# Performance work log

Measured on AMD Instinct MI355X. Metric: run time of the kernel, lower is better.

Reference implementation:

```python
import jax, jax.numpy as jnp
import numpy as np

ALPHA = 0.5
SPLIT_RATIO = 0.5
NUM_HEADS = 12
LN_EPS = 1e-6


def _layernorm(x, g, b):
    m = x.mean(-1, keepdims=True)
    v = ((x - m) ** 2).mean(-1, keepdims=True)
    return (x - m) * jax.lax.rsqrt(v + LN_EPS) * g + b


def setup_inputs() -> dict:
    key = jax.random.key(0)
    ks = jax.random.split(key, 8)
    B, N1, C, L, Hm = 16, 197, 768, 4, 3072
    s = 0.02
    return {
        "x": jax.random.normal(ks[0], (B, N1, C), jnp.float32),
        "glb_cls_attn": jax.random.uniform(ks[1], (B, N1 - 1), jnp.float32),
        "split_w": jax.random.normal(ks[2], (C, 4 * C), jnp.float32) * s,
        "split_b": jnp.zeros((4 * C,), jnp.float32),
        "ln1_g": jnp.ones((L, C), jnp.float32),
        "ln1_b": jnp.zeros((L, C), jnp.float32),
        "qkv_w": jax.random.normal(ks[3], (L, C, 3 * C), jnp.float32) * s,
        "qkv_b": jnp.zeros((L, 3 * C), jnp.float32),
        "proj_w": jax.random.normal(ks[4], (L, C, C), jnp.float32) * s,
        "proj_b": jnp.zeros((L, C), jnp.float32),
        "ln2_g": jnp.ones((L, C), jnp.float32),
        "ln2_b": jnp.zeros((L, C), jnp.float32),
        "fc1_w": jax.random.normal(ks[5], (L, C, Hm), jnp.float32) * s,
        "fc1_b": jnp.zeros((L, Hm), jnp.float32),
        "fc2_w": jax.random.normal(ks[6], (L, Hm, C), jnp.float32) * s,
        "fc2_b": jnp.zeros((L, C), jnp.float32),
    }


def reference(x, glb_cls_attn, split_w, split_b, ln1_g, ln1_b, qkv_w, qkv_b,
              proj_w, proj_b, ln2_g, ln2_b, fc1_w, fc1_b, fc2_w, fc2_b):
    B, _, C = x.shape
    H = NUM_HEADS
    D = C // H
    scale = D ** -0.5

    # --- token split based on global cls attention importance ---
    cls_tok, tokens = x[:, :1], x[:, 1:]
    order = jnp.argsort(-glb_cls_attn, axis=1)  # descending importance
    tokens = jnp.take_along_axis(tokens, order[:, :, None], axis=1)
    n = tokens.shape[1]
    split_n = int(n * SPLIT_RATIO)
    st = tokens[:, :split_n] @ split_w + split_b          # [B, split_n, 4C]
    st = st.reshape(B, split_n * 4, C)                    # each token -> 4 tokens
    x = jnp.concatenate([cls_tok, st, tokens[:, split_n:]], axis=1)
    N = x.shape[1]
    glb = jnp.zeros((B, N - 1), x.dtype)

    def block(carry, p):
        x, g = carry
        g1, b1, qw, qb, pw, pb, g2, b2, w1, bb1, w2, bb2 = p
        h = _layernorm(x, g1, b1)
        qkv = (h @ qw + qb).reshape(B, N, 3, H, D).transpose(2, 0, 3, 1, 4)
        q, k, v = qkv[0], qkv[1], qkv[2]                  # [B,H,N,D]
        attn = jax.nn.softmax(jnp.einsum('bhnd,bhmd->bhnm', q, k) * scale, axis=-1)
        cls_attn = attn[:, :, 0, 1:].mean(axis=1)         # mean over heads, row 0
        o = jnp.einsum('bhnm,bhmd->bhnd', attn, v).transpose(0, 2, 1, 3).reshape(B, N, C)
        x = x + o @ pw + pb
        h2 = _layernorm(x, g2, b2)
        x = x + jax.nn.gelu(h2 @ w1 + bb1, approximate=False) @ w2 + bb2
        g = ALPHA * g + (1.0 - ALPHA) * cls_attn
        return (x, g), None

    (x, glb), _ = jax.lax.scan(
        block, (x, glb),
        (ln1_g, ln1_b, qkv_w, qkv_b, proj_w, proj_b,
         ln2_g, ln2_b, fc1_w, fc1_b, fc2_w, fc2_b))
    return x, glb
```

## Files before the change

kernel.cpp:

```cpp
#include <hip/hip_runtime.h>
#include <math.h>

typedef unsigned short u16;
typedef short s16x8 __attribute__((ext_vector_type(8)));
typedef float f32x4 __attribute__((ext_vector_type(4)));

#define BB 16
#define N1 197
#define NTOK 196
#define SPLITN 98
#define NN 491
#define CC 768
#define H3 2304
#define HM 3072
#define NH 12
#define NL 4
#define BN (BB*NN)
#define MSPLIT (BB*SPLITN)

__device__ __forceinline__ float b2f(u16 u) {
    union { unsigned int i; float f; } x; x.i = ((unsigned int)u) << 16; return x.f;
}
__device__ __forceinline__ u16 f2b(float f) {
    union { float f; unsigned int i; } x; x.f = f;
    unsigned int i = x.i;
    return (u16)((i + 0x7fffu + ((i >> 16) & 1u)) >> 16);
}
__device__ __forceinline__ float ldx(const void* p, long long i, int isf32) {
    return isf32 ? ((const float*)p)[i] : b2f(((const u16*)p)[i]);
}

__device__ __forceinline__ float gelu_fast(float v) {
    float x = v * 0.70710678118654752f;
    float ax = fabsf(x);
    float t = __builtin_amdgcn_rcpf(fmaf(0.3275911f, ax, 1.0f));
    float p = t * fmaf(t, fmaf(t, fmaf(t, fmaf(t, 1.061405429f, -1.453152027f),
                                       1.421413741f), -0.284496736f), 0.254829592f);
    float e = __expf(-ax * ax);
    float er = fmaf(-p, e, 1.0f);
    er = copysignf(er, x);
    return 0.5f * v * (1.0f + er);
}

__device__ __forceinline__ void gload_lds16(const u16* g, u16* l) {
    __builtin_amdgcn_global_load_lds(
        (const __attribute__((address_space(1))) unsigned int*)g,
        (__attribute__((address_space(3))) unsigned int*)l,
        16, 0, 0);
}

__global__ void detect_k(const void* __restrict__ ln1_g, int* __restrict__ flag) {
    unsigned int w = ((const unsigned int*)ln1_g)[0];
    *flag = (w == 0x3F800000u) ? 1 : 0;
}

__global__ void zero_out_k(u16* __restrict__ out, long long n) {
    long long idx = (long long)blockIdx.x * 256 + threadIdx.x;
    if (idx < n) out[idx] = 0;
}

__global__ void zero_glb_k(float* __restrict__ glb) {
    int idx = blockIdx.x * 256 + threadIdx.x;
    if (idx < BB * (NN - 1)) glb[idx] = 0.0f;
}

__global__ void sort_k(const void* __restrict__ g, int* __restrict__ order,
                       const int* __restrict__ dflag) {
    __shared__ float v[256];
    int isf32 = *dflag;
    int b = blockIdx.x, t = threadIdx.x;
    float vv = -1e30f;
    if (t < NTOK) {
        vv = ldx(g, (long long)b * NTOK + t, isf32);
        if (!(vv == vv)) vv = -1e30f;
    }
    v[t] = vv;
    __syncthreads();
    if (t < NTOK) {
        float mv = v[t]; int r = 0;
        for (int j = 0; j < NTOK; j++) {
            float vj = v[j];
            if (vj > mv || (vj == mv && j < t)) r++;
        }
        order[b * NTOK + r] = t;
    }
}

__device__ __forceinline__ int clamp_tok(int tok) {
    return (tok < 0) ? 0 : (tok > NTOK - 1 ? NTOK - 1 : tok);
}

__global__ void gather_split_k(const void* __restrict__ x_in, const int* __restrict__ order,
                               u16* __restrict__ Asp, const int* __restrict__ dflag) {
    int isf32 = *dflag;
    long long idx = (long long)blockIdx.x * 256 + threadIdx.x;
    if (idx >= (long long)MSPLIT * CC) return;
    int c = (int)(idx % CC); int m = (int)(idx / CC); int b = m / SPLITN, r = m % SPLITN;
    int tok = clamp_tok(order[b * NTOK + r]);
    Asp[idx] = f2b(ldx(x_in, ((long long)b * N1 + 1 + tok) * CC + c, isf32));
}

__global__ void build_x_k(const void* __restrict__ x_in, const u16* __restrict__ st,
                          const int* __restrict__ order, float* __restrict__ x,
                          const int* __restrict__ dflag) {
    int isf32 = *dflag;
    long long idx = (long long)blockIdx.x * 256 + threadIdx.x;
    if (idx >= (long long)BN * CC) return;
    int c = (int)(idx % CC);
    int m = (int)(idx / CC);
    int b = m / NN, pos = m % NN;
    float v;
    if (pos == 0) {
        v = ldx(x_in, (long long)b * N1 * CC + c, isf32);
    } else if (pos < 1 + 4 * SPLITN) {
        int tt = pos - 1; int r = tt >> 2, kq = tt & 3;
        v = b2f(st[((long long)b * SPLITN + r) * HM + kq * CC + c]);
    } else {
        int j = pos - (1 + 4 * SPLITN);
        int tok = clamp_tok(order[b * NTOK + SPLITN + j]);
        v = ldx(x_in, ((long long)b * N1 + 1 + tok) * CC + c, isf32);
    }
    x[idx] = v;
}

__global__ void transpose_off_k(const void* __restrict__ in, u16* __restrict__ out, int K, int N,
                                long long off, const int* __restrict__ dflag) {
    __shared__ u16 tile[32][33];
    int isf32 = *dflag;
    int n0 = blockIdx.x * 32, k0 = blockIdx.y * 32;
    int tx = threadIdx.x, ty = threadIdx.y;
    for (int i = ty; i < 32; i += 8)
        tile[i][tx] = f2b(ldx(in, off + (long long)(k0 + i) * N + n0 + tx, isf32));
    __syncthreads();
    for (int i = ty; i < 32; i += 8) out[(long long)(n0 + i) * K + k0 + tx] = tile[tx][i];
}

__global__ __launch_bounds__(256) void ln_k(const float* __restrict__ x, const void* __restrict__ g,
                                            const void* __restrict__ bgain, u16* __restrict__ h,
                                            int goff, const int* __restrict__ dflag) {
    __shared__ float sb[8];
    int isf32 = *dflag;
    int row = blockIdx.x, t = threadIdx.x;
    const float* xr = x + (long long)row * CC;
    float v0 = xr[t], v1 = xr[t + 256], v2 = xr[t + 512];
    float s = v0 + v1 + v2;
    for (int o = 32; o > 0; o >>= 1) s += __shfl_down(s, o, 64);
    int lane = t & 63, w = t >> 6;
    if (lane == 0) sb[w] = s;
    __syncthreads();
    float mean = (sb[0] + sb[1] + sb[2] + sb[3]) * (1.0f / 768.0f);
    float d0 = v0 - mean, d1 = v1 - mean, d2 = v2 - mean;
    float q = d0 * d0 + d1 * d1 + d2 * d2;
    for (int o = 32; o > 0; o >>= 1) q += __shfl_down(q, o, 64);
    if (lane == 0) sb[4 + w] = q;
    __syncthreads();
    float var = (sb[4] + sb[5] + sb[6] + sb[7]) * (1.0f / 768.0f);
    float rs = rsqrtf(var + 1e-6f);
    long long o0 = (long long)row * CC;
    h[o0 + t]       = f2b(d0 * rs * ldx(g, goff + t, isf32)       + ldx(bgain, goff + t, isf32));
    h[o0 + t + 256] = f2b(d1 * rs * ldx(g, goff + t + 256, isf32) + ldx(bgain, goff + t + 256, isf32));
    h[o0 + t + 512] = f2b(d2 * rs * ldx(g, goff + t + 512, isf32) + ldx(bgain, goff + t + 512, isf32));
}

template<int TBM, int TBN>
__global__ __launch_bounds__(256) void gemm_t(const u16* __restrict__ A, const u16* __restrict__ BT,
                                              const void* __restrict__ bias, int boff,
                                              void* __restrict__ out,
                                              int M, int N, int K, int mode,
                                              const int* __restrict__ dflag) {
    constexpr int WM = TBM / 2, WN = TBN / 2, FM = WM / 16, FN = WN / 16;
    constexpr int AI = TBM / 64;
    constexpr int BI = TBN / 64;
    constexpr int LPS = AI + BI;
    __shared__ __align__(16) u16 As[3][TBM * 32];
    __shared__ __align__(16) u16 Bs[3][TBN * 32];
    int isf32 = *dflag;

    int gx = gridDim.x, gy = gridDim.y;
    int nwg = gx * gy;
    int bid0 = blockIdx.y * gx + blockIdx.x;
    int q = nwg >> 3, rr = nwg & 7;
    int xcd = bid0 & 7, sl = bid0 >> 3;
    int wg = (xcd < rr ? xcd * (q + 1) : rr * (q + 1) + (xcd - rr) * q) + sl;
    int by = wg % gy, bx = wg / gy;
    int m0 = bx * TBM, n0 = by * TBN;

    int t = threadIdx.x, wave = t >> 6, lane = t & 63;
    int wm = (wave >> 1) * WM, wn = (wave & 1) * WN;
    int fr = lane & 15, quad = lane >> 4;

    int srow = lane >> 2;
    int scol = ((lane & 3) ^ ((srow >> 1) & 3)) * 8;

    long long aoff[AI];
    long long bofs[BI];
#pragma unroll
    for (int i = 0; i < AI; i++) {
        int r0 = wave * (TBM / 4) + i * 16;
        int row = m0 + r0 + srow;
        if (row > M - 1) row = M - 1;
        aoff[i] = (long long)row * K + scol;
    }
#pragma unroll
    for (int i = 0; i < BI; i++) {
        int r0 = wave * (TBN / 4) + i * 16;
        bofs[i] = (long long)(n0 + r0 + srow) * K + scol;
    }

    f32x4 acc[FM][FN];
#pragma unroll
    for (int i = 0; i < FM; i++)
#pragma unroll
        for (int j = 0; j < FN; j++) acc[i][j] = (f32x4){0.f, 0.f, 0.f, 0.f};

    const int nk = K >> 5;

#define STAGE(BUF, KT) do {                                                          \
        int k0_ = (KT) << 5;                                                         \
        _Pragma("unroll") for (int i = 0; i < AI; i++)                               \
            gload_lds16(&A[aoff[i] + k0_], &As[BUF][(wave * (TBM / 4) + i * 16) * 32]); \
        _Pragma("unroll") for (int i = 0; i < BI; i++)                               \
            gload_lds16(&BT[bofs[i] + k0_], &Bs[BUF][(wave * (TBN / 4) + i * 16) * 32]); \
    } while (0)

#define WAITP(PF) do {                                                               \
        if (PF) {                                                                    \
            if constexpr (LPS == 4)      asm volatile("s_waitcnt vmcnt(4)" ::: "memory"); \
            else if constexpr (LPS == 3) asm volatile("s_waitcnt vmcnt(3)" ::: "memory"); \
            else                         asm volatile("s_waitcnt vmcnt(2)" ::: "memory"); \
        } else                           asm volatile("s_waitcnt vmcnt(0)" ::: "memory"); \
    } while (0)

    STAGE(0, 0);
    if (nk > 1) STAGE(1, 1);
    WAITP(nk > 1);
    __builtin_amdgcn_sched_barrier(0);
    __builtin_amdgcn_s_barrier();
    __builtin_amdgcn_sched_barrier(0);

    int rofs = ((quad ^ ((fr >> 1) & 3)) * 8);

#define GSTEP(BUF, PFBUF) {                                                          \
        bool pf_ = (kt + 2 < nk);                                                    \
        if (pf_) STAGE(PFBUF, kt + 2);               \
        s16x8 af_[FM], bf_[FN];                                                      \
        _Pragma("unroll") for (int i = 0; i < FM; i++)                               \
            af_[i] = *(const s16x8*)&As[BUF][(wm + i * 16 + fr) * 32 + rofs];        \
        _Pragma("unroll") for (int j = 0; j < FN; j++)                               \
            bf_[j] = *(const s16x8*)&Bs[BUF][(wn + j * 16 + fr) * 32 + rofs];        \
        _Pragma("unroll") for (int i = 0; i < FM; i++)                               \
            _Pragma("unroll") for (int j = 0; j < FN; j++)                           \
                acc[i][j] = __builtin_amdgcn_mfma_f32_16x16x32_bf16(af_[i], bf_[j], acc[i][j], 0, 0, 0); \
        if (kt + 1 < nk) {                                                           \
            WAITP(pf_);                               \
            __builtin_amdgcn_sched_barrier(0);                                       \
            __builtin_amdgcn_s_barrier();                 \
            __builtin_amdgcn_sched_barrier(0);                                       \
        }                                                                            \
        kt++;                                                                        \
    }

    int kt = 0;
    while (kt < nk) {
        GSTEP(0, 2)
        if (kt < nk) GSTEP(1, 0)
        if (kt < nk) GSTEP(2, 1)
    }
#undef GSTEP
#undef WAITP
#undef STAGE

#pragma unroll
    for (int i = 0; i < FM; i++) {
#pragma unroll
        for (int j = 0; j < FN; j++) {
#pragma unroll
            for (int r = 0; r < 4; r++) {
                int row = m0 + wm + i * 16 + quad * 4 + r;
                int col = n0 + wn + j * 16 + fr;
                if (row < M) {
                    float v = acc[i][j][r] + ldx(bias, boff + col, isf32);
                    long long idx = (long long)row * N + col;
                    if (mode == 1) ((u16*)out)[idx] = f2b(v);
                    else if (mode == 2) ((u16*)out)[idx] = f2b(gelu_fast(v));
                    else ((float*)out)[idx] += v;
                }
            }
        }
    }
}

__global__ __launch_bounds__(256, 2) void attn_mfma_k(const u16* __restrict__ qkv,
                                                      u16* __restrict__ o,
                                                      float* __restrict__ cls_partial, int b0,
                                                      int nbh) {
    int bid = blockIdx.x;
    int chunk = nbh >> 3;
    int xcd = bid & 7, s = bid >> 3;
    int qt = s & 7;
    int bh = xcd * chunk + (s >> 3);
    int lb = bh / NH, h = bh % NH;
    int i0 = qt * 64;
    int w = threadIdx.x >> 6, lane = threadIdx.x & 63;
    int fr = lane & 15, quad = lane >> 4;
    int fk = quad * 8;

    __shared__ __align__(16) u16 Qs[64][72];
    __shared__ __align__(16) u16 Ks[64][72];
    __shared__ __align__(16) u16 Vt[64][72];
    __shared__ __align__(16) u16 Pst[4][16][72];

    const long long rowbase = (long long)lb * NN * H3 + (long long)h * 64;

    {
        int t = threadIdx.x;
#pragma unroll
        for (int i = 0; i < 2; i++) {
            int e = t + i * 256;
            int r = e >> 3, c8 = (e & 7) * 8;
            uint4 v = make_uint4(0u, 0u, 0u, 0u);
            int qrow = i0 + r;
            if (qrow < NN) v = *(const uint4*)&qkv[rowbase + (long long)qrow * H3 + c8];
            *(uint4*)&Qs[r][c8] = v;
        }
    }
    __syncthreads();
    s16x8 aq0 = *(const s16x8*)&Qs[w * 16 + fr][fk];
    s16x8 aq1 = *(const s16x8*)&Qs[w * 16 + fr][32 + fk];

    f32x4 S[32];
#pragma unroll
    for (int i = 0; i < 32; i++) S[i] = (f32x4){0.f, 0.f, 0.f, 0.f};

#pragma unroll
    for (int kt = 0; kt < 8; kt++) {
        int tb = kt * 64;
        __syncthreads();
        {
            int t = threadIdx.x;
#pragma unroll
            for (int i = 0; i < 2; i++) {
                int e = t + i * 256;
                int r = e >> 3, c8 = (e & 7) * 8;
                uint4 v = make_uint4(0u, 0u, 0u, 0u);
                int krow = tb + r;
                if (krow < NN) v = *(const uint4*)&qkv[rowbase + (long long)krow * H3 + CC + c8];
                *(uint4*)&Ks[r][c8] = v;
            }
        }
        __syncthreads();
#pragma unroll
        for (int ct = 0; ct < 4; ct++) {
            s16x8 bk0 = *(const s16x8*)&Ks[ct * 16 + fr][fk];
            s16x8 bk1 = *(const s16x8*)&Ks[ct * 16 + fr][32 + fk];
            S[kt * 4 + ct] = __builtin_amdgcn_mfma_f32_16x16x32_bf16(aq0, bk0, S[kt * 4 + ct], 0, 0, 0);
            S[kt * 4 + ct] = __builtin_amdgcn_mfma_f32_16x16x32_bf16(aq1, bk1, S[kt * 4 + ct], 0, 0, 0);
        }
    }

    float mrow[4] = {-1e30f, -1e30f, -1e30f, -1e30f};
#pragma unroll
    for (int tl = 0; tl < 32; tl++) {
        int col = tl * 16 + fr;
        bool valid = col < NN;
#pragma unroll
        for (int r = 0; r < 4; r++) {
            float s2 = S[tl][r] * 0.125f;
            s2 = valid ? s2 : -1e30f;
            S[tl][r] = s2;
            mrow[r] = fmaxf(mrow[r], s2);
        }
    }
#pragma unroll
    for (int m = 1; m < 16; m <<= 1)
#pragma unroll
        for (int r = 0; r < 4; r++) mrow[r] = fmaxf(mrow[r], __shfl_xor(mrow[r], m, 64));
    float lrow[4] = {0.f, 0.f, 0.f, 0.f};
#pragma unroll
    for (int tl = 0; tl < 32; tl++)
#pragma unroll
        for (int r = 0; r < 4; r++) {
            float e = __expf(S[tl][r] - mrow[r]);
            S[tl][r] = e;
            lrow[r] += e;
        }
#pragma unroll
    for (int m = 1; m < 16; m <<= 1)
#pragma unroll
        for (int r = 0; r < 4; r++) lrow[r] += __shfl_xor(lrow[r], m, 64);
    float linv[4];
#pragma unroll
    for (int r = 0; r < 4; r++) linv[r] = 1.0f / lrow[r];

    if (qt == 0 && w == 0 && quad == 0) {
        long long cbase = (long long)((b0 + lb) * NH + h) * (NN - 1);
        float inv = linv[0];
#pragma unroll
        for (int tl = 0; tl < 32; tl++) {
            int col = tl * 16 + fr;
            if (col >= 1 && col < NN) cls_partial[cbase + col - 1] = S[tl][0] * inv;
        }
    }

    f32x4 O[4];
#pragma unroll
    for (int d = 0; d < 4; d++) O[d] = (f32x4){0.f, 0.f, 0.f, 0.f};
#pragma unroll
    for (int kt2 = 0; kt2 < 8; kt2++) {
        int vb = kt2 * 64;
        __syncthreads();
        {
            int t = threadIdx.x;
#pragma unroll
            for (int i = 0; i < 2; i++) {
                int e = t + i * 256;
                int r = e >> 3, c8 = (e & 7) * 8;
                uint4 v = make_uint4(0u, 0u, 0u, 0u);
                int vrow = vb + r;
                if (vrow < NN) v = *(const uint4*)&qkv[rowbase + (long long)vrow * H3 + 2 * CC + c8];
                union { uint4 u; u16 e8[8]; } tmp; tmp.u = v;
                int rblk = r >> 3, rin = r & 7;
#pragma unroll
                for (int j = 0; j < 8; j++) {
                    int row = c8 + j;
                    int cp = ((rblk ^ (row >> 3)) << 3) | rin;
                    Vt[row][cp] = tmp.e8[j];
                }
            }
        }
#pragma unroll
        for (int tt = 0; tt < 4; tt++) {
            int tl = kt2 * 4 + tt;
#pragma unroll
            for (int r = 0; r < 4; r++)
                Pst[w][quad * 4 + r][tt * 16 + fr] = f2b(S[tl][r]);
        }
        __syncthreads();
        s16x8 ap0 = *(const s16x8*)&Pst[w][fr][fk];
        s16x8 ap1 = *(const s16x8*)&Pst[w][fr][32 + fk];
#pragma unroll
        for (int dt = 0; dt < 4; dt++) {
            int row = dt * 16 + fr;
            int g = row >> 3;
            s16x8 bv0 = *(const s16x8*)&Vt[row][((quad ^ g) & 7) * 8];
            s16x8 bv1 = *(const s16x8*)&Vt[row][(((4 + quad) ^ g) & 7) * 8];
            O[dt] = __builtin_amdgcn_mfma_f32_16x16x32_bf16(ap0, bv0, O[dt], 0, 0, 0);
            O[dt] = __builtin_amdgcn_mfma_f32_16x16x32_bf16(ap1, bv1, O[dt], 0, 0, 0);
        }
    }

#pragma unroll
    for (int r = 0; r < 4; r++) {
        int qrow = i0 + w * 16 + quad * 4 + r;
        if (qrow < NN) {
            long long obase = ((long long)(b0 + lb) * NN + qrow) * CC + h * 64;
#pragma unroll
            for (int dt = 0; dt < 4; dt++)
                o[obase + dt * 16 + fr] = f2b(O[dt][r] * linv[r]);
        }
    }
}

__global__ void glb_update_k(const float* __restrict__ cls_partial, float* __restrict__ glb) {
    int idx = blockIdx.x * 256 + threadIdx.x;
    if (idx >= BB * (NN - 1)) return;
    int b = idx / (NN - 1), j = idx % (NN - 1);
    float s = 0;
    for (int h = 0; h < NH; h++) s += cls_partial[(long long)(b * NH + h) * (NN - 1) + j];
    glb[idx] = 0.5f * glb[idx] + 0.5f * (s / NH);
}

__global__ void finalize_k(const float* __restrict__ x, const float* __restrict__ glb,
                           void* __restrict__ out, const int* __restrict__ dflag) {
    int isf32 = *dflag;
    long long nx = (long long)BN * CC;
    long long nt = nx + (long long)BB * (NN - 1);
    long long idx = (long long)blockIdx.x * 256 + threadIdx.x;
    if (idx >= nt) return;
    float v = (idx < nx) ? x[idx] : glb[idx - nx];
    if (isf32) ((float*)out)[idx] = v;
    else ((u16*)out)[idx] = f2b(v);
}

static inline char* carve(char*& p, size_t bytes) {
    char* r = p;
    p += (bytes + 255) & ~(size_t)255;
    return r;
}
static inline size_t padb(size_t b) { return (b + 255) & ~(size_t)255; }

extern "C" void kernel_launch(void* const* d_in, const int* in_sizes, int n_in,
                              void* d_out, int out_size, void* d_ws, size_t ws_size,
                              hipStream_t stream) {
    const void* x_in    = d_in[0];
    const void* glb_in  = d_in[1];
    const void* split_w = d_in[2];
    const void* split_b = d_in[3];
    const void* ln1_g   = d_in[4];
    const void* ln1_b   = d_in[5];
    const void* qkv_w   = d_in[6];
    const void* qkv_b   = d_in[7];
    const void* proj_w  = d_in[8];
    const void* proj_b  = d_in[9];
    const void* ln2_g   = d_in[10];
    const void* ln2_b   = d_in[11];
    const void* fc1_w   = d_in[12];
    const void* fc1_b   = d_in[13];
    const void* fc2_w   = d_in[14];
    const void* fc2_b   = d_in[15];

    const size_t sz_x    = (size_t)BN * CC * 4;
    const size_t sz_h    = (size_t)BN * CC * 2;
    const size_t sz_wt   = (size_t)HM * CC * 2;
    const size_t sz_cls  = (size_t)BB * NH * (NN - 1) * 4;
    const size_t sz_glb  = (size_t)BB * (NN - 1) * 4;
    const size_t sz_ord  = (size_t)BB * NTOK * 4;

    const size_t rA2 = (size_t)BN * HM * 2;
    const size_t rA  = (size_t)BN * H3 * 2;
    const size_t rB  = (size_t)(BN / 4) * HM * 2;
    const size_t rC  = (size_t)MSPLIT * HM * 2;

    const size_t base = padb(sz_x) + padb(sz_h) + 2 * padb(sz_wt) + padb(sz_cls) +
                        padb(sz_glb) + padb(sz_ord) + 256;
    int tier; size_t rsz;
    if (ws_size >= base + padb(rA2))     { tier = 0; rsz = rA2; }
    else if (ws_size >= base + padb(rA)) { tier = 1; rsz = rA; }
    else if (ws_size >= base + padb(rB)) { tier = 2; rsz = rB; }
    else if (ws_size >= base + padb(rC)) { tier = 3; rsz = rC; }
    else {
        zero_out_k<<<(int)(((long long)out_size + 255) / 256), 256, 0, stream>>>((u16*)d_out, (long long)out_size);
        return;
    }

    char* p = (char*)d_ws;
    float* x_f32   = (float*)carve(p, sz_x);
    u16* h_buf     = (u16*)carve(p, sz_h);
    u16* region1   = (u16*)carve(p, rsz);
    u16* wtA       = (u16*)carve(p, sz_wt);
    u16* wtB       = (u16*)carve(p, sz_wt);
    float* cls_par = (float*)carve(p, sz_cls);
    float* glb_f32 = (float*)carve(p, sz_glb);
    int* order     = (int*)carve(p, sz_ord);
    int* dflag     = (int*)carve(p, 256);
    u16* Asp       = wtB;

    auto gemm = [&](const u16* A, const u16* BT, const void* bias, int boff, void* out,
                    int M, int N, int K, int mode) {
        long long b128 = (long long)((M + 127) / 128) * (N / 128);
        if ((N & 127) == 0 && b128 >= 512)
            gemm_t<128, 128><<<dim3((M + 127) / 128, N / 128), 256, 0, stream>>>(
                A, BT, bias, boff, out, M, N, K, mode, dflag);
        else if ((N & 63) == 0)
            gemm_t<128, 64><<<dim3((M + 127) / 128, N / 64), 256, 0, stream>>>(
                A, BT, bias, boff, out, M, N, K, mode, dflag);
        else
            gemm_t<64, 64><<<dim3((M + 63) / 64, N / 64), 256, 0, stream>>>(
                A, BT, bias, boff, out, M, N, K, mode, dflag);
    };

    dim3 tb(32, 8);
    detect_k<<<1, 1, 0, stream>>>(ln1_g, dflag);
    zero_glb_k<<<(BB * (NN - 1) + 255) / 256, 256, 0, stream>>>(glb_f32);
    sort_k<<<BB, 256, 0, stream>>>(glb_in, order, dflag);
    gather_split_k<<<(MSPLIT * CC + 255) / 256, 256, 0, stream>>>(x_in, order, Asp, dflag);
    transpose_off_k<<<dim3(HM / 32, CC / 32), tb, 0, stream>>>(split_w, wtA, CC, HM, 0, dflag);
    gemm(Asp, wtA, split_b, 0, region1, MSPLIT, HM, CC, 1);
    build_x_k<<<(int)(((long long)BN * CC + 255) / 256), 256, 0, stream>>>(x_in, region1, order,
                                                                           x_f32, dflag);

    const int bch  = (tier <= 1) ? BB : 4;
    const int nbch = BB / bch;
    const int matt = bch * NN;
    const int nbh  = bch * NH;
    const int nmch = (tier == 0) ? 1 : (tier == 1) ? 2 : (tier == 2) ? 4 : 8;
    const int mch  = BN / nmch;

    for (int l = 0; l < NL; l++) {
        transpose_off_k<<<dim3(H3 / 32, CC / 32), tb, 0, stream>>>(qkv_w, wtA, CC, H3,
                                                                   (long long)l * CC * H3, dflag);
        ln_k<<<BN, 256, 0, stream>>>(x_f32, ln1_g, ln1_b, h_buf, l * CC, dflag);
        for (int bc = 0; bc < nbch; bc++) {
            const u16* Ain = h_buf + (long long)bc * matt * CC;
            gemm(Ain, wtA, qkv_b, l * H3, region1, matt, H3, CC, 1);
            attn_mfma_k<<<dim3(nbh * 8), 256, 0, stream>>>(region1, h_buf, cls_par, bc * bch, nbh);
        }
        glb_update_k<<<(BB * (NN - 1) + 255) / 256, 256, 0, stream>>>(cls_par, glb_f32);
        transpose_off_k<<<dim3(CC / 32, CC / 32), tb, 0, stream>>>(proj_w, wtA, CC, CC,
                                                                   (long long)l * CC * CC, dflag);
        gemm(h_buf, wtA, proj_b, l * CC, x_f32, BN, CC, CC, 3);
        ln_k<<<BN, 256, 0, stream>>>(x_f32, ln2_g, ln2_b, h_buf, l * CC, dflag);
        transpose_off_k<<<dim3(HM / 32, CC / 32), tb, 0, stream>>>(fc1_w, wtA, CC, HM,
                                                                   (long long)l * CC * HM, dflag);
        transpose_off_k<<<dim3(CC / 32, HM / 32), tb, 0, stream>>>(fc2_w, wtB, HM, CC,
                                                                   (long long)l * HM * CC, dflag);
        for (int mc = 0; mc < nmch; mc++) {
            const u16* Ain = h_buf + (long long)mc * mch * CC;
            float* xout    = x_f32 + (long long)mc * mch * CC;
            gemm(Ain, wtA, fc1_b, l * HM, region1, mch, HM, CC, 2);
            gemm(region1, wtB, fc2_b, l * CC, xout, mch, CC, HM, 3);
        }
    }
    long long total_out = (long long)BN * CC + (long long)BB * (NN - 1);
    finalize_k<<<(int)((total_out + 255) / 256), 256, 0, stream>>>(x_f32, glb_f32, d_out, dflag);
}
```

Measured before the change: 1.659 ms.

## Vectorize weight transpose with 64x64 tiles, hoist GEMM bias loads, tune launch bounds

Replaces the 32x32 scalar weight transpose with a 64x64 tile kernel that loads float4 or uint4 rows and writes 16-element vectors per thread, cutting the number of memory transactions in the per-layer weight conversions. The GEMM gets a launch-bounds occupancy hint of 2 blocks per CU. It also drops one scheduling barrier before each s_barrier and hoists the bias loads out of the epilogue loop. The occupancy hint can force register spilling, and relaxed scheduling barriers could change instruction interleaving.

```diff
diff --git a/kernel.cpp b/kernel.cpp
--- a/kernel.cpp
+++ b/kernel.cpp
@@ -123,16 +123,43 @@
     x[idx] = v;
 }
 
-__global__ void transpose_off_k(const void* __restrict__ in, u16* __restrict__ out, int K, int N,
-                                long long off, const int* __restrict__ dflag) {
-    __shared__ u16 tile[32][33];
+__global__ __launch_bounds__(256) void transpose64_k(const void* __restrict__ in,
+                                                     u16* __restrict__ out, int K, int N,
+                                                     long long off,
+                                                     const int* __restrict__ dflag) {
+    __shared__ __align__(16) u16 tile[64][72];
     int isf32 = *dflag;
-    int n0 = blockIdx.x * 32, k0 = blockIdx.y * 32;
-    int tx = threadIdx.x, ty = threadIdx.y;
-    for (int i = ty; i < 32; i += 8)
-        tile[i][tx] = f2b(ldx(in, off + (long long)(k0 + i) * N + n0 + tx, isf32));
+    int n0 = blockIdx.x * 64, k0 = blockIdx.y * 64;
+    int t = threadIdx.x;
+    if (isf32) {
+        int r = t >> 4, c = (t & 15) * 4;
+        const float* src = (const float*)in + off;
+#pragma unroll
+        for (int i = 0; i < 4; i++) {
+            int row = k0 + r + i * 16;
+            float4 v = *(const float4*)&src[(long long)row * N + n0 + c];
+            ushort4 u;
+            u.x = f2b(v.x); u.y = f2b(v.y); u.z = f2b(v.z); u.w = f2b(v.w);
+            *(ushort4*)&tile[r + i * 16][c] = u;
+        }
+    } else {
+        int r = t >> 3, c = (t & 7) * 8;
+        const u16* src = (const u16*)in + off;
+#pragma unroll
+        for (int i = 0; i < 2; i++) {
+            int row = k0 + r + i * 32;
+            uint4 v = *(const uint4*)&src[(long long)row * N + n0 + c];
+            *(uint4*)&tile[r + i * 32][c] = v;
+        }
+    }
     __syncthreads();
-    for (int i = ty; i < 32; i += 8) out[(long long)(n0 + i) * K + k0 + tx] = tile[tx][i];
+    int j = t >> 2, c2 = (t & 3) * 16;
+    __attribute__((aligned(16))) u16 buf[16];
+#pragma unroll
+    for (int m = 0; m < 16; m++) buf[m] = tile[c2 + m][j];
+    long long ob = (long long)(n0 + j) * K + k0 + c2;
+    *(uint4*)&out[ob]     = *(const uint4*)&buf[0];
+    *(uint4*)&out[ob + 8] = *(const uint4*)&buf[8];
 }
 
 __global__ __launch_bounds__(256) void ln_k(const float* __restrict__ x, const void* __restrict__ g,
@@ -163,11 +190,11 @@
 }
 
 template<int TBM, int TBN>
-__global__ __launch_bounds__(256) void gemm_t(const u16* __restrict__ A, const u16* __restrict__ BT,
-                                              const void* __restrict__ bias, int boff,
-                                              void* __restrict__ out,
-                                              int M, int N, int K, int mode,
-                                              const int* __restrict__ dflag) {
+__global__ __launch_bounds__(256, 2) void gemm_t(const u16* __restrict__ A, const u16* __restrict__ BT,
+                                                 const void* __restrict__ bias, int boff,
+                                                 void* __restrict__ out,
+                                                 int M, int N, int K, int mode,
+                                                 const int* __restrict__ dflag) {
     constexpr int WM = TBM / 2, WN = TBN / 2, FM = WM / 16, FN = WN / 16;
     constexpr int AI = TBM / 64;
     constexpr int BI = TBN / 64;
@@ -234,7 +261,6 @@
     STAGE(0, 0);
     if (nk > 1) STAGE(1, 1);
     WAITP(nk > 1);
-    __builtin_amdgcn_sched_barrier(0);
     __builtin_amdgcn_s_barrier();
     __builtin_amdgcn_sched_barrier(0);
 
@@ -253,7 +279,6 @@
                 acc[i][j] = __builtin_amdgcn_mfma_f32_16x16x32_bf16(af_[i], bf_[j], acc[i][j], 0, 0, 0); \
         if (kt + 1 < nk) {                                                           \
             WAITP(pf_);                               \
-            __builtin_amdgcn_sched_barrier(0);                                       \
             __builtin_amdgcn_s_barrier();                 \
             __builtin_amdgcn_sched_barrier(0);                                       \
         }                                                                            \
@@ -270,6 +295,10 @@
 #undef WAITP
 #undef STAGE
 
+    float bv[FN];
+#pragma unroll
+    for (int j = 0; j < FN; j++) bv[j] = ldx(bias, boff + n0 + wn + j * 16 + fr, isf32);
+
 #pragma unroll
     for (int i = 0; i < FM; i++) {
 #pragma unroll
@@ -279,7 +308,7 @@
                 int row = m0 + wm + i * 16 + quad * 4 + r;
                 int col = n0 + wn + j * 16 + fr;
                 if (row < M) {
-                    float v = acc[i][j][r] + ldx(bias, boff + col, isf32);
+                    float v = acc[i][j][r] + bv[j];
                     long long idx = (long long)row * N + col;
                     if (mode == 1) ((u16*)out)[idx] = f2b(v);
                     else if (mode == 2) ((u16*)out)[idx] = f2b(gelu_fast(v));
@@ -559,12 +588,11 @@
                 A, BT, bias, boff, out, M, N, K, mode, dflag);
     };
 
-    dim3 tb(32, 8);
     detect_k<<<1, 1, 0, stream>>>(ln1_g, dflag);
     zero_glb_k<<<(BB * (NN - 1) + 255) / 256, 256, 0, stream>>>(glb_f32);
     sort_k<<<BB, 256, 0, stream>>>(glb_in, order, dflag);
     gather_split_k<<<(MSPLIT * CC + 255) / 256, 256, 0, stream>>>(x_in, order, Asp, dflag);
-    transpose_off_k<<<dim3(HM / 32, CC / 32), tb, 0, stream>>>(split_w, wtA, CC, HM, 0, dflag);
+    transpose64_k<<<dim3(HM / 64, CC / 64), 256, 0, stream>>>(split_w, wtA, CC, HM, 0, dflag);
     gemm(Asp, wtA, split_b, 0, region1, MSPLIT, HM, CC, 1);
     build_x_k<<<(int)(((long long)BN * CC + 255) / 256), 256, 0, stream>>>(x_in, region1, order,
                                                                            x_f32, dflag);
@@ -577,8 +605,8 @@
     const int mch  = BN / nmch;
 
     for (int l = 0; l < NL; l++) {
-        transpose_off_k<<<dim3(H3 / 32, CC / 32), tb, 0, stream>>>(qkv_w, wtA, CC, H3,
-                                                                   (long long)l * CC * H3, dflag);
+        transpose64_k<<<dim3(H3 / 64, CC / 64), 256, 0, stream>>>(qkv_w, wtA, CC, H3,
+                                                                  (long long)l * CC * H3, dflag);
         ln_k<<<BN, 256, 0, stream>>>(x_f32, ln1_g, ln1_b, h_buf, l * CC, dflag);
         for (int bc = 0; bc < nbch; bc++) {
             const u16* Ain = h_buf + (long long)bc * matt * CC;
@@ -586,14 +614,14 @@
             attn_mfma_k<<<dim3(nbh * 8), 256, 0, stream>>>(region1, h_buf, cls_par, bc * bch, nbh);
         }
         glb_update_k<<<(BB * (NN - 1) + 255) / 256, 256, 0, stream>>>(cls_par, glb_f32);
-        transpose_off_k<<<dim3(CC / 32, CC / 32), tb, 0, stream>>>(proj_w, wtA, CC, CC,
-                                                                   (long long)l * CC * CC, dflag);
+        transpose64_k<<<dim3(CC / 64, CC / 64), 256, 0, stream>>>(proj_w, wtA, CC, CC,
+                                                                  (long long)l * CC * CC, dflag);
         gemm(h_buf, wtA, proj_b, l * CC, x_f32, BN, CC, CC, 3);
         ln_k<<<BN, 256, 0, stream>>>(x_f32, ln2_g, ln2_b, h_buf, l * CC, dflag);
-        transpose_off_k<<<dim3(HM / 32, CC / 32), tb, 0, stream>>>(fc1_w, wtA, CC, HM,
-                                                                   (long long)l * CC * HM, dflag);
-        transpose_off_k<<<dim3(CC / 32, HM / 32), tb, 0, stream>>>(fc2_w, wtB, HM, CC,
-                                                                   (long long)l * HM * CC, dflag);
+        transpose64_k<<<dim3(HM / 64, CC / 64), 256, 0, stream>>>(fc1_w, wtA, CC, HM,
+                                                                  (long long)l * CC * HM, dflag);
+        transpose64_k<<<dim3(CC / 64, HM / 64), 256, 0, stream>>>(fc2_w, wtB, HM, CC,
+                                                                  (long long)l * HM * CC, dflag);
         for (int mc = 0; mc < nmch; mc++) {
             const u16* Ain = h_buf + (long long)mc * mch * CC;
             float* xout    = x_f32 + (long long)mc * mch * CC;
```

Measured after the change: 1.577 ms. 4.9% less time.
